# Kernel tuning notes

Measured on AMD Instinct MI355X. Metric: run time of the kernel, lower is better.

## Reference

```python
import jax, jax.numpy as jnp
import numpy as np

N = 100000
E = 1600000
D = 128  # out_dim == head_dim (num_heads = 1)


def setup_inputs() -> dict:
    key = jax.random.key(0)
    ks = jax.random.split(key, 16)
    s = 0.05
    inp = {
        "h": jax.random.normal(ks[0], (N, D), dtype=jnp.float32),
        "c": jax.random.normal(ks[1], (N, 3), dtype=jnp.float32),
        "src": jax.random.randint(ks[2], (E,), 0, N),
        "dst": jax.random.randint(ks[3], (E,), 0, N),
        # Q/K/V projections (use_bias=False)
        "Wq": jax.random.normal(ks[4], (D, D), dtype=jnp.float32) * s,
        "Wk": jax.random.normal(ks[5], (D, D), dtype=jnp.float32) * s,
        "Wv": jax.random.normal(ks[6], (D, D), dtype=jnp.float32) * s,
        # linear_p: Linear(3,3) -> ReLU -> Linear(3,D)
        "Wp1": jax.random.normal(ks[7], (3, 3), dtype=jnp.float32) * s,
        "bp1": jnp.zeros((3,), dtype=jnp.float32),
        "Wp2": jax.random.normal(ks[8], (3, D), dtype=jnp.float32) * s,
        "bp2": jnp.zeros((D,), dtype=jnp.float32),
        # edge MLP: Linear(D,D) -> ReLU -> Linear(D,1)
        "We1": jax.random.normal(ks[9], (D, D), dtype=jnp.float32) * s,
        "be1": jnp.zeros((D,), dtype=jnp.float32),
        "We2": jax.random.normal(ks[10], (D, 1), dtype=jnp.float32) * s,
        "be2": jnp.zeros((1,), dtype=jnp.float32),
        # output projection O (has bias)
        "Wo": jax.random.normal(ks[11], (D, D), dtype=jnp.float32) * s,
        "bo": jnp.zeros((D,), dtype=jnp.float32),
    }
    return inp


def reference(h, c, src, dst, Wq, Wk, Wv, Wp1, bp1, Wp2, bp2,
              We1, be1, We2, be2, Wo, bo):
    scale = np.sqrt(np.float32(D))  # sqrt(out_dim) used by scaled_exp
    n = h.shape[0]
    # node projections
    Q = h @ Wq                                   # [N, D]
    K = h @ Wk                                   # [N, D]
    V = h @ Wv                                   # [N, D]
    P = jax.nn.relu(c @ Wp1 + bp1) @ Wp2 + bp2   # [N, D] position encoding
    # per-edge point-transformer score: MLP(K[src] - Q[dst] + P[src])
    dif = K[src] - Q[dst] + P[src]               # [E, D]
    raw = jax.nn.relu(dif @ We1 + be1) @ We2 + be2  # [E, 1]
    score = jnp.exp(jnp.clip(raw / scale, -5.0, 5.0))  # [E, 1]
    # gather-multiply-scatter: weighted V+P sum and normalizer z per dst node
    msg = (V + P)[src] * score                   # [E, D]
    wV = jax.ops.segment_sum(msg, dst, num_segments=n)    # [N, D]
    z = jax.ops.segment_sum(score, dst, num_segments=n)   # [N, 1]
    head_out = wV / z                            # [N, D]
    return head_out @ Wo + bo                    # [N, D]
```

## Files before the change

### kernel.cpp

```cpp
#include <hip/hip_runtime.h>
#include <math.h>

#define DD 128
#define CAP 10240
typedef unsigned int u32;
typedef unsigned short u16;
typedef __attribute__((ext_vector_type(8))) short bf16x8;
typedef __attribute__((ext_vector_type(4))) float f32x4;
typedef __attribute__((ext_vector_type(2))) float f32x2;

__device__ __forceinline__ float4 f4zero() { return make_float4(0.f, 0.f, 0.f, 0.f); }
__device__ __forceinline__ u32 bf16rne(float f) {
    u32 u = __float_as_uint(f);
    u += 0x7FFFu + ((u >> 16) & 1u);
    return u >> 16;
}
__device__ __forceinline__ u32 pack2(float lo, float hi) {
    return bf16rne(lo) | (bf16rne(hi) << 16);
}
__device__ __forceinline__ float unlo(u32 u) { return __uint_as_float(u << 16); }
__device__ __forceinline__ float unhi(u32 u) { return __uint_as_float(u & 0xFFFF0000u); }

__global__ __launch_bounds__(256) void fused_pre(
    const float* __restrict__ Wq, const float* __restrict__ Wk,
    const float* __restrict__ Wv, const float* __restrict__ We1,
    const float* __restrict__ be1, const float* __restrict__ Wp2,
    const float* __restrict__ bp2, const float* __restrict__ Wo,
    u32* __restrict__ BF,
    const int* __restrict__ src, const int* __restrict__ dst,
    int* __restrict__ gcount, u32* __restrict__ ebuf, int E) {
    const int t = threadIdx.x;
    if (blockIdx.x < 30) {
        const int bid = blockIdx.x * 4 + (t >> 6);
        const int l = t & 63;
        const int c = l & 15;
        const int kg = l >> 4;
        float val[8];

        const int ct = bid / 5, ks = bid - ct * 5;
        const int u = ct / 6, r = ct - u * 6;
        const int n = 32 * u + 16 * (r < 2 ? r : (r & 1)) + c;
#pragma unroll
        for (int j = 0; j < 8; ++j) {
            const int k = ks * 32 + kg * 8 + j;
            float v = 0.f;
            if (r < 2) {
                if (k < 128) {
                    float a = 0.f;
                    for (int q = 0; q < 128; ++q)
                        a = fmaf(Wq[k * 128 + q], We1[q * 128 + n], a);
                    v = a;
                }
            } else if (r < 4) {
                if (k < 128) {
                    float a = 0.f;
                    for (int q = 0; q < 128; ++q)
                        a = fmaf(Wk[k * 128 + q], We1[q * 128 + n], a);
                    v = a;
                } else if (k < 131) {
                    float a = 0.f;
                    for (int q = 0; q < 128; ++q)
                        a = fmaf(Wp2[(k - 128) * 128 + q], We1[q * 128 + n], a);
                    v = a;
                } else if (k == 131) {
                    float a = be1[n];
                    for (int q = 0; q < 128; ++q)
                        a = fmaf(bp2[q], We1[q * 128 + n], a);
                    v = a;
                }
            } else {
                if (k < 128) {
                    float a = 0.f;
                    for (int q = 0; q < 128; ++q)
                        a = fmaf(Wv[k * 128 + q], Wo[q * 128 + n], a);
                    v = a;
                } else if (k < 131) {
                    float a = 0.f;
                    for (int q = 0; q < 128; ++q)
                        a = fmaf(Wp2[(k - 128) * 128 + q], Wo[q * 128 + n], a);
                    v = a;
                } else if (k == 131) {
                    float a = 0.f;
                    for (int q = 0; q < 128; ++q)
                        a = fmaf(bp2[q], Wo[q * 128 + n], a);
                    v = a;
                }
            }
            val[j] = v;
        }
        u32* dp = &BF[((size_t)bid * 64 + l) * 4];
        dp[0] = pack2(val[0], val[1]);
        dp[1] = pack2(val[2], val[3]);
        dp[2] = pack2(val[4], val[5]);
        dp[3] = pack2(val[6], val[7]);
    } else {
        __shared__ int hist[256];
        __shared__ int base[256];
        hist[t] = 0;
        __syncthreads();
        const int chunk = (blockIdx.x - 30) * 4096;
        int bk[16], rk[16];
        u32 pv[16];
#pragma unroll
        for (int i = 0; i < 16; ++i) {
            int idx = chunk + i * 256 + t;
            bk[i] = -1;
            if (idx < E) {
                int dd = dst[idx];
                int ss = src[idx];
                bk[i] = dd >> 9;
                pv[i] = ((u32)ss << 9) | (u32)(dd & 511);
                rk[i] = atomicAdd(&hist[bk[i]], 1);
            }
        }
        __syncthreads();
        if (hist[t]) base[t] = t * CAP + atomicAdd(&gcount[t], hist[t]);
        __syncthreads();
#pragma unroll
        for (int i = 0; i < 16; ++i) {
            if (bk[i] >= 0) ebuf[base[bk[i]] + rk[i]] = pv[i];
        }
    }
}

__global__ __launch_bounds__(256) void scanB_we2r(
    const int* __restrict__ gcount, int* __restrict__ bucket_base,
    const float* __restrict__ We2, float* __restrict__ We2r) {
    __shared__ int s[256];
    int t = threadIdx.x;
    int orig = gcount[t];
    s[t] = orig;
    __syncthreads();
    for (int off = 1; off < 256; off <<= 1) {
        int x = (t >= off) ? s[t - off] : 0;
        __syncthreads();
        s[t] += x;
        __syncthreads();
    }
    bucket_base[t] = s[t] - orig;
    if (t < 128) {
        int col = 32 * (t >> 5) + 16 * (t & 1) + ((t & 31) >> 1);
        We2r[t] = We2[col];
    }
}

__global__ __launch_bounds__(256) void fused_mid(
    const float* __restrict__ h, const float* __restrict__ c,
    const float* __restrict__ Wp1, const float* __restrict__ bp1,
    const u32* __restrict__ BF,
    u32* __restrict__ QWb, unsigned char* __restrict__ KV, int N,
    const int* __restrict__ gcount, const int* __restrict__ bucket_base,
    const u32* __restrict__ ebuf, int* __restrict__ ssrc,
    int* __restrict__ offs, int E, int NR) {
    __shared__ u32 lds[64 * 96];
    const int t = threadIdx.x;

    if ((int)blockIdx.x < NR) {
        int* cnt = (int*)lds;
        int* cur = cnt + 512;
        int* ts = cur + 512;
        const int r = blockIdx.x;
        const int cnt_r = gcount[r];
        const int base_r = bucket_base[r];
        cnt[t] = 0;
        cnt[t + 256] = 0;
        __syncthreads();
        const u32* eb = &ebuf[(size_t)r * CAP];
        for (int i = t; i < cnt_r; i += 256) atomicAdd(&cnt[eb[i] & 511], 1);
        __syncthreads();
        int v0 = cnt[2 * t], v1 = cnt[2 * t + 1];
        int pair = v0 + v1;
        ts[t] = pair;
        __syncthreads();
        for (int off = 1; off < 256; off <<= 1) {
            int x = (t >= off) ? ts[t - off] : 0;
            __syncthreads();
            ts[t] += x;
            __syncthreads();
        }
        int ex = ts[t] - pair;
        cur[2 * t] = ex;
        cur[2 * t + 1] = ex + v0;
        offs[r * 512 + 2 * t] = base_r + ex;
        offs[r * 512 + 2 * t + 1] = base_r + ex + v0;
        if (r == NR - 1 && t == 255) offs[NR * 512] = E;
        __syncthreads();
        for (int i = t; i < cnt_r; i += 256) {
            u32 e = eb[i];
            int p = atomicAdd(&cur[e & 511], 1);
            ssrc[base_r + p] = (int)(e >> 9);
        }
    } else {
        u32* hs = lds;
        const int row0 = ((int)blockIdx.x - NR) * 64;

#pragma unroll
        for (int i = 0; i < 8; ++i) {
            int f = t + i * 256;
            int row = f >> 5;
            int cq = f & 31;
            float4 v = f4zero();
            if (row0 + row < N) v = *(const float4*)&h[(size_t)(row0 + row) * DD + cq * 4];
            int idx = row * 96 + ((cq * 2) ^ ((row & 7) << 2));
            uint2 p;
            p.x = pack2(v.x, v.y);
            p.y = pack2(v.z, v.w);
            *(uint2*)&hs[idx] = p;
        }
        if (t < 64) {
            int row = t;
            float u0 = 0.f, u1 = 0.f, u2 = 0.f;
            if (row0 + row < N) {
                const float* cr = &c[(size_t)(row0 + row) * 3];
                float c0 = cr[0], c1 = cr[1], c2 = cr[2];
                u0 = fmaxf(bp1[0] + c0 * Wp1[0] + c1 * Wp1[3] + c2 * Wp1[6], 0.f);
                u1 = fmaxf(bp1[1] + c0 * Wp1[1] + c1 * Wp1[4] + c2 * Wp1[7], 0.f);
                u2 = fmaxf(bp1[2] + c0 * Wp1[2] + c1 * Wp1[5] + c2 * Wp1[8], 0.f);
            }
            int swz = (row & 7) << 2;
            uint4 z0 = make_uint4(pack2(u0, u1), pack2(u2, 1.0f), 0u, 0u);
            uint4 zz = make_uint4(0u, 0u, 0u, 0u);
#pragma unroll
            for (int q = 0; q < 4; ++q) {
                int idx = row * 96 + 64 + ((q * 4) ^ swz);
                *(uint4*)&hs[idx] = (q == 0) ? z0 : zz;
            }
        }
        __syncthreads();

        const int w = t >> 6, l = t & 63;
        const int cc = l & 15, kg = l >> 4;

        f32x4 acc[4][6];
#pragma unroll
        for (int rt = 0; rt < 4; ++rt)
#pragma unroll
            for (int r = 0; r < 6; ++r) acc[rt][r] = (f32x4){0.f, 0.f, 0.f, 0.f};

#pragma unroll
        for (int ks = 0; ks < 5; ++ks) {
            bf16x8 a[4];
#pragma unroll
            for (int rt = 0; rt < 4; ++rt) {
                int row = rt * 16 + cc;
                int idx = row * 96 + ((ks * 16 + kg * 4) ^ ((row & 7) << 2));
                a[rt] = *(const bf16x8*)&hs[idx];
            }
#pragma unroll
            for (int r = 0; r < 6; ++r) {
                const bf16x8 b = *(const bf16x8*)&BF[(((size_t)(w * 6 + r) * 5 + ks) * 64 + l) * 4];
#pragma unroll
                for (int rt = 0; rt < 4; ++rt)
                    acc[rt][r] = __builtin_amdgcn_mfma_f32_16x16x32_bf16(a[rt], b, acc[rt][r], 0, 0, 0);
            }
        }

#pragma unroll
        for (int rt = 0; rt < 4; ++rt) {
#pragma unroll
            for (int j = 0; j < 4; ++j) {
                int row = row0 + rt * 16 + kg * 4 + j;
                if (row >= N) continue;
                QWb[(size_t)row * 64 + w * 16 + cc] = pack2(acc[rt][0][j], acc[rt][1][j]);
                unsigned char* kvrow = &KV[(size_t)row * 384];
                u32 kp = __builtin_amdgcn_cvt_pk_fp8_f32(acc[rt][2][j], acc[rt][3][j], 0u, false);
                *(u16*)&kvrow[w * 32 + cc * 2] = (u16)kp;
                *(u32*)&kvrow[128 + 4 * (w * 16 + cc)] = pack2(acc[rt][4][j], acc[rt][5][j]);
            }
        }
    }
}

__global__ __launch_bounds__(256) void aggregate(
    const int* __restrict__ offs, const int* __restrict__ ssrc,
    const unsigned char* __restrict__ KV, const u32* __restrict__ QWb,
    const float* __restrict__ We2r, const float* __restrict__ be2,
    const float* __restrict__ bo, float* __restrict__ out, int N) {
    const int node = (blockIdx.x * 256 + threadIdx.x) >> 6;
    const int lane = threadIdx.x & 63;
    if (node >= N) return;
    const int g = lane >> 4, i = lane & 15;

    const float SC = 0.08838834764831845f * 1.4426950408889634f;
    const float CL = 5.0f * 1.4426950408889634f;

    uint4 Qu = *(const uint4*)&QWb[(size_t)node * 64 + 4 * i];
    f32x2 q01 = {unlo(Qu.x), unhi(Qu.x)};
    f32x2 q23 = {unlo(Qu.y), unhi(Qu.y)};
    f32x2 q45 = {unlo(Qu.z), unhi(Qu.z)};
    f32x2 q67 = {unlo(Qu.w), unhi(Qu.w)};
    f32x2 w01 = *(const f32x2*)&We2r[8 * i];
    f32x2 w23 = *(const f32x2*)&We2r[8 * i + 2];
    f32x2 w45 = *(const f32x2*)&We2r[8 * i + 4];
    f32x2 w67 = *(const f32x2*)&We2r[8 * i + 6];
    const float B2SC = be2[0] * SC;
    const f32x2 zero2 = {0.f, 0.f};

    const int beg = offs[node], end = offs[node + 1];
    f32x2 acc01 = zero2, acc23 = zero2, acc45 = zero2, acc67 = zero2;
    float zacc = 0.f;

    int e = beg + g;
    int s = (e < end) ? ssrc[e] : 0;
    for (int e0 = beg; e0 < end; e0 += 4) {
        const bool act = (e0 + g) < end;
        const unsigned char* row = &KV[(size_t)s * 384];
        uint2 kk = *(const uint2*)&row[8 * i];
        uint4 vv = *(const uint4*)&row[128 + 16 * i];
        int en = e0 + 4 + g;
        s = (en < end) ? ssrc[en] : 0;

        f32x2 d, p2;
        d = __builtin_amdgcn_cvt_pk_f32_fp8(kk.x, false) - q01;
        d = __builtin_elementwise_max(d, zero2);
        p2 = d * w01;
        d = __builtin_amdgcn_cvt_pk_f32_fp8(kk.x, true) - q23;
        d = __builtin_elementwise_max(d, zero2);
        p2 += d * w23;
        d = __builtin_amdgcn_cvt_pk_f32_fp8(kk.y, false) - q45;
        d = __builtin_elementwise_max(d, zero2);
        p2 += d * w45;
        d = __builtin_amdgcn_cvt_pk_f32_fp8(kk.y, true) - q67;
        d = __builtin_elementwise_max(d, zero2);
        p2 += d * w67;
        float p = p2[0] + p2[1];
#pragma unroll
        for (int off = 1; off <= 8; off <<= 1) p += __shfl_xor(p, off);

        float targ = fmaf(p, SC, B2SC);
        targ = fminf(fmaxf(targ, -CL), CL);
        float sc = act ? exp2f(targ) : 0.f;
        f32x2 sc2 = {sc, sc};

        f32x2 v;
        v = (f32x2){unlo(vv.x), unhi(vv.x)}; acc01 += v * sc2;
        v = (f32x2){unlo(vv.y), unhi(vv.y)}; acc23 += v * sc2;
        v = (f32x2){unlo(vv.z), unhi(vv.z)}; acc45 += v * sc2;
        v = (f32x2){unlo(vv.w), unhi(vv.w)}; acc67 += v * sc2;
        zacc += sc;
    }

    float a0 = acc01[0], a1 = acc01[1], a2 = acc23[0], a3 = acc23[1];
    float a4 = acc45[0], a5 = acc45[1], a6 = acc67[0], a7 = acc67[1];

    a0 += __shfl_xor(a0, 16); a0 += __shfl_xor(a0, 32);
    a1 += __shfl_xor(a1, 16); a1 += __shfl_xor(a1, 32);
    a2 += __shfl_xor(a2, 16); a2 += __shfl_xor(a2, 32);
    a3 += __shfl_xor(a3, 16); a3 += __shfl_xor(a3, 32);
    a4 += __shfl_xor(a4, 16); a4 += __shfl_xor(a4, 32);
    a5 += __shfl_xor(a5, 16); a5 += __shfl_xor(a5, 32);
    a6 += __shfl_xor(a6, 16); a6 += __shfl_xor(a6, 32);
    a7 += __shfl_xor(a7, 16); a7 += __shfl_xor(a7, 32);
    zacc += __shfl_xor(zacc, 16); zacc += __shfl_xor(zacc, 32);

    if (g == 0) {
        float rz = 1.0f / zacc;
        const int base = 32 * (i >> 2) + 4 * (i & 3);
        float4 bA = *(const float4*)&bo[base];
        float4 bB = *(const float4*)&bo[base + 16];
        float4 oA = make_float4(fmaf(a0, rz, bA.x), fmaf(a2, rz, bA.y),
                                fmaf(a4, rz, bA.z), fmaf(a6, rz, bA.w));
        float4 oB = make_float4(fmaf(a1, rz, bB.x), fmaf(a3, rz, bB.y),
                                fmaf(a5, rz, bB.z), fmaf(a7, rz, bB.w));
        float* orow = &out[(size_t)node * DD];
        *(float4*)&orow[base] = oA;
        *(float4*)&orow[base + 16] = oB;
    }
}

extern "C" void kernel_launch(void* const* d_in, const int* in_sizes, int n_in,
                              void* d_out, int out_size, void* d_ws, size_t ws_size,
                              hipStream_t stream) {
    const float* h   = (const float*)d_in[0];
    const float* c   = (const float*)d_in[1];
    const int*   src = (const int*)d_in[2];
    const int*   dst = (const int*)d_in[3];
    const float* Wq  = (const float*)d_in[4];
    const float* Wk  = (const float*)d_in[5];
    const float* Wv  = (const float*)d_in[6];
    const float* Wp1 = (const float*)d_in[7];
    const float* bp1 = (const float*)d_in[8];
    const float* Wp2 = (const float*)d_in[9];
    const float* bp2 = (const float*)d_in[10];
    const float* We1 = (const float*)d_in[11];
    const float* be1 = (const float*)d_in[12];
    const float* We2 = (const float*)d_in[13];
    const float* be2 = (const float*)d_in[14];
    const float* Wo  = (const float*)d_in[15];
    const float* bo  = (const float*)d_in[16];

    const int N = in_sizes[0] / DD;
    const int E = in_sizes[2];
    const int NR = (N + 511) >> 9;
    const int NB1 = (E + 4095) / 4096;
    const int NG = (N + 63) / 64;

    u32* BF    = (u32*)d_ws;
    u32* QWb   = BF + 120 * 256;
    unsigned char* KV = (unsigned char*)(QWb + (size_t)N * 64);
    int* offs  = (int*)(KV + (size_t)N * 384);
    int* gcount = offs + ((size_t)NR * 512 + 1);
    int* bbase  = gcount + 256;
    float* We2r = (float*)(bbase + 256);
    int* ssrc   = (int*)(We2r + 128);
    u32* ebuf   = (u32*)(ssrc + E);

    hipMemsetAsync(gcount, 0, 256 * sizeof(int), stream);

    fused_pre<<<30 + NB1, 256, 0, stream>>>(Wq, Wk, Wv, We1, be1, Wp2, bp2, Wo,
                                            BF, src, dst, gcount, ebuf, E);

    scanB_we2r<<<1, 256, 0, stream>>>(gcount, bbase, We2, We2r);

    fused_mid<<<NR + NG, 256, 0, stream>>>(
        h, c, Wp1, bp1, BF, QWb, KV, N,
        gcount, bbase, ebuf, ssrc, offs, E, NR);

    aggregate<<<(N * 64 + 255) / 256, 256, 0, stream>>>(
        offs, ssrc, KV, QWb, We2r, be2, bo, (float*)d_out, N);
}
```

Before: 195.8 us.

## Quantize per-node V rows to int8 with per-row scale to shrink gathered KV

Stores the V (Wo-folded) part of each node's KV row as offset-int8 with a per-row float scale instead of bf16, shrinking the row stride from 384 to 272 bytes. The scale comes from a shared-memory atomicMax row reduction in the projection kernel. The aggregate kernel dequantizes by folding the scale into the score weight and subtracting a 128*sum correction at the end. This cuts gathered bytes per edge in the memory-bound aggregation, but loses precision on V and adds an extra scalar load per edge plus two block syncs in the producer.

```diff
diff --git a/kernel.cpp b/kernel.cpp
--- a/kernel.cpp
+++ b/kernel.cpp
@@ -3,6 +3,7 @@
 
 #define DD 128
 #define CAP 10240
+#define KVS 272
 typedef unsigned int u32;
 typedef unsigned short u16;
 typedef __attribute__((ext_vector_type(8))) short bf16x8;
@@ -20,6 +21,10 @@
 }
 __device__ __forceinline__ float unlo(u32 u) { return __uint_as_float(u << 16); }
 __device__ __forceinline__ float unhi(u32 u) { return __uint_as_float(u & 0xFFFF0000u); }
+__device__ __forceinline__ float ub0(u32 v) { return (float)(v & 0xFFu); }
+__device__ __forceinline__ float ub1(u32 v) { return (float)((v >> 8) & 0xFFu); }
+__device__ __forceinline__ float ub2(u32 v) { return (float)((v >> 16) & 0xFFu); }
+__device__ __forceinline__ float ub3(u32 v) { return (float)(v >> 24); }
 
 __global__ __launch_bounds__(256) void fused_pre(
     const float* __restrict__ Wq, const float* __restrict__ Wk,
@@ -255,17 +260,38 @@
             }
         }
 
+        __syncthreads();
+        if (t < 64) hs[t] = 0u;
+        __syncthreads();
 #pragma unroll
         for (int rt = 0; rt < 4; ++rt) {
 #pragma unroll
             for (int j = 0; j < 4; ++j) {
-                int row = row0 + rt * 16 + kg * 4 + j;
+                int rl = rt * 16 + kg * 4 + j;
+                float m = fmaxf(fabsf(acc[rt][4][j]), fabsf(acc[rt][5][j]));
+                atomicMax((int*)&hs[rl], __float_as_int(m));
+            }
+        }
+        __syncthreads();
+
+#pragma unroll
+        for (int rt = 0; rt < 4; ++rt) {
+#pragma unroll
+            for (int j = 0; j < 4; ++j) {
+                int rl = rt * 16 + kg * 4 + j;
+                int row = row0 + rl;
                 if (row >= N) continue;
+                float smax = __int_as_float((int)hs[rl]);
+                float scale = (smax > 0.f) ? smax * (1.0f / 127.0f) : 1.0f;
+                float rsc = 1.0f / scale;
                 QWb[(size_t)row * 64 + w * 16 + cc] = pack2(acc[rt][0][j], acc[rt][1][j]);
-                unsigned char* kvrow = &KV[(size_t)row * 384];
+                unsigned char* kvrow = &KV[(size_t)row * KVS];
                 u32 kp = __builtin_amdgcn_cvt_pk_fp8_f32(acc[rt][2][j], acc[rt][3][j], 0u, false);
                 *(u16*)&kvrow[w * 32 + cc * 2] = (u16)kp;
-                *(u32*)&kvrow[128 + 4 * (w * 16 + cc)] = pack2(acc[rt][4][j], acc[rt][5][j]);
+                int q0 = (int)rintf(acc[rt][4][j] * rsc) + 128;
+                int q1 = (int)rintf(acc[rt][5][j] * rsc) + 128;
+                *(u16*)&kvrow[128 + 2 * (w * 16 + cc)] = (u16)((q0 & 0xFF) | ((q1 & 0xFF) << 8));
+                if (w == 0 && cc == 0) *(float*)&kvrow[256] = scale;
             }
         }
     }
@@ -297,16 +323,18 @@
     const f32x2 zero2 = {0.f, 0.f};
 
     const int beg = offs[node], end = offs[node + 1];
-    f32x2 acc01 = zero2, acc23 = zero2, acc45 = zero2, acc67 = zero2;
-    float zacc = 0.f;
+    float a0 = 0.f, a1 = 0.f, a2 = 0.f, a3 = 0.f;
+    float a4 = 0.f, a5 = 0.f, a6 = 0.f, a7 = 0.f;
+    float zacc = 0.f, zs = 0.f;
 
     int e = beg + g;
     int s = (e < end) ? ssrc[e] : 0;
     for (int e0 = beg; e0 < end; e0 += 4) {
         const bool act = (e0 + g) < end;
-        const unsigned char* row = &KV[(size_t)s * 384];
+        const unsigned char* row = &KV[(size_t)s * KVS];
         uint2 kk = *(const uint2*)&row[8 * i];
-        uint4 vv = *(const uint4*)&row[128 + 16 * i];
+        uint2 vv = *(const uint2*)&row[128 + 8 * i];
+        float scl = *(const float*)&row[256];
         int en = e0 + 4 + g;
         s = (en < end) ? ssrc[en] : 0;
 
@@ -330,18 +358,19 @@
         float targ = fmaf(p, SC, B2SC);
         targ = fminf(fmaxf(targ, -CL), CL);
         float sc = act ? exp2f(targ) : 0.f;
-        f32x2 sc2 = {sc, sc};
-
-        f32x2 v;
-        v = (f32x2){unlo(vv.x), unhi(vv.x)}; acc01 += v * sc2;
-        v = (f32x2){unlo(vv.y), unhi(vv.y)}; acc23 += v * sc2;
-        v = (f32x2){unlo(vv.z), unhi(vv.z)}; acc45 += v * sc2;
-        v = (f32x2){unlo(vv.w), unhi(vv.w)}; acc67 += v * sc2;
+        float scsc = sc * scl;
         zacc += sc;
-    }
-
-    float a0 = acc01[0], a1 = acc01[1], a2 = acc23[0], a3 = acc23[1];
-    float a4 = acc45[0], a5 = acc45[1], a6 = acc67[0], a7 = acc67[1];
+        zs += scsc;
+
+        a0 = fmaf(ub0(vv.x), scsc, a0);
+        a1 = fmaf(ub1(vv.x), scsc, a1);
+        a2 = fmaf(ub2(vv.x), scsc, a2);
+        a3 = fmaf(ub3(vv.x), scsc, a3);
+        a4 = fmaf(ub0(vv.y), scsc, a4);
+        a5 = fmaf(ub1(vv.y), scsc, a5);
+        a6 = fmaf(ub2(vv.y), scsc, a6);
+        a7 = fmaf(ub3(vv.y), scsc, a7);
+    }
 
     a0 += __shfl_xor(a0, 16); a0 += __shfl_xor(a0, 32);
     a1 += __shfl_xor(a1, 16); a1 += __shfl_xor(a1, 32);
@@ -352,16 +381,18 @@
     a6 += __shfl_xor(a6, 16); a6 += __shfl_xor(a6, 32);
     a7 += __shfl_xor(a7, 16); a7 += __shfl_xor(a7, 32);
     zacc += __shfl_xor(zacc, 16); zacc += __shfl_xor(zacc, 32);
+    zs += __shfl_xor(zs, 16); zs += __shfl_xor(zs, 32);
 
     if (g == 0) {
+        float corr = 128.0f * zs;
         float rz = 1.0f / zacc;
         const int base = 32 * (i >> 2) + 4 * (i & 3);
         float4 bA = *(const float4*)&bo[base];
         float4 bB = *(const float4*)&bo[base + 16];
-        float4 oA = make_float4(fmaf(a0, rz, bA.x), fmaf(a2, rz, bA.y),
-                                fmaf(a4, rz, bA.z), fmaf(a6, rz, bA.w));
-        float4 oB = make_float4(fmaf(a1, rz, bB.x), fmaf(a3, rz, bB.y),
-                                fmaf(a5, rz, bB.z), fmaf(a7, rz, bB.w));
+        float4 oA = make_float4(fmaf(a0 - corr, rz, bA.x), fmaf(a2 - corr, rz, bA.y),
+                                fmaf(a4 - corr, rz, bA.z), fmaf(a6 - corr, rz, bA.w));
+        float4 oB = make_float4(fmaf(a1 - corr, rz, bB.x), fmaf(a3 - corr, rz, bB.y),
+                                fmaf(a5 - corr, rz, bB.z), fmaf(a7 - corr, rz, bB.w));
         float* orow = &out[(size_t)node * DD];
         *(float4*)&orow[base] = oA;
         *(float4*)&orow[base + 16] = oB;
@@ -398,7 +429,7 @@
     u32* BF    = (u32*)d_ws;
     u32* QWb   = BF + 120 * 256;
     unsigned char* KV = (unsigned char*)(QWb + (size_t)N * 64);
-    int* offs  = (int*)(KV + (size_t)N * 384);
+    int* offs  = (int*)(KV + (size_t)N * KVS);
     int* gcount = offs + ((size_t)NR * 512 + 1);
     int* bbase  = gcount + 256;
     float* We2r = (float*)(bbase + 256);
```

New measurement: 203.4 us. 3.9% more time.
